# Kernel optimization log

Measured on AMD Instinct MI355X. Metric: run time of the kernel, lower is better.

## Reference

```python
import jax, jax.numpy as jnp
import numpy as np

N_QUBITS = 8
N_WORDS = 16
DEGREE = 3
N_ANSATZ_LAYERS = 2
VOCAB = 50257
EMB = 512
BATCH = 16
N_ROTS = 4 * N_QUBITS * N_ANSATZ_LAYERS  # 64
DIM = 2 ** N_QUBITS


def _ry_mat(th):
    # [[cos, -sin],[sin, cos]] on theta/2, batched over leading dim
    c = jnp.cos(th / 2).astype(jnp.complex64)
    s = jnp.sin(th / 2).astype(jnp.complex64)
    return jnp.stack([jnp.stack([c, -s], -1), jnp.stack([s, c], -1)], -2)


def _rx_mat(th):
    # [[cos, -i sin],[-i sin, cos]] on theta/2
    c = jnp.cos(th / 2).astype(jnp.complex64)
    s = jnp.sin(th / 2).astype(jnp.complex64)
    return jnp.stack([jnp.stack([c, -1j * s], -1), jnp.stack([-1j * s, c], -1)], -2)


def _apply_1q(st, M, w):
    # st: [BB, 2^n] complex, M: [BB,2,2]; wire 0 is the most-significant axis (tq convention)
    BB = st.shape[0]
    s = st.reshape(BB, 2 ** w, 2, -1)
    s = jnp.einsum('bij,bljr->blir', M, s)
    return s.reshape(BB, -1)


def _apply_ctrl(st, M, c, t, n):
    # controlled-1q gate: apply M on target t only in the control=1 subspace
    BB = st.shape[0]
    full = st.reshape((BB,) + (2,) * n)
    s0 = jnp.take(full, 0, axis=c + 1)
    s1 = jnp.take(full, 1, axis=c + 1)
    ta = (t if t < c else t - 1) + 1  # target axis after removing control axis
    s1 = jnp.moveaxis(s1, ta, -1)
    s1 = jnp.einsum('bij,b...j->b...i', M, s1)
    s1 = jnp.moveaxis(s1, -1, ta)
    return jnp.stack([s0, s1], axis=c + 1).reshape(BB, -1)


def _sim14(st, params, n, layers):
    # circuit-14 ansatz: ry ring, crx down-ring, ry ring, crx up-ring (per layer)
    idx = 0
    for _ in range(layers):
        for i in range(n):
            st = _apply_1q(st, _ry_mat(params[:, idx]), i); idx += 1
        for i in range(n - 1, -1, -1):
            st = _apply_ctrl(st, _rx_mat(params[:, idx]), i, (i + 1) % n, n); idx += 1
        for i in range(n):
            st = _apply_1q(st, _ry_mat(params[:, idx]), i); idx += 1
        for i in [n - 1] + list(range(n - 1)):
            st = _apply_ctrl(st, _rx_mat(params[:, idx]), i, (i - 1) % n, n); idx += 1
    return st


def _apply_unitaries(base, wparams, coeffs):
    # base: [B, DIM]; wparams: [B, W, N_ROTS]; coeffs: [B, W] complex -> LCU sum_w c_w U_w |psi>
    B, W = wparams.shape[0], wparams.shape[1]
    rep = jnp.repeat(base, W, axis=0)  # matches torch repeat(1,W).view(-1,DIM)
    st = _sim14(rep, wparams.reshape(B * W, -1), N_QUBITS, N_ANSATZ_LAYERS)
    return jnp.einsum('bwi,bw->bi', st.reshape(B, W, DIM), coeffs)


def _measure_xyz(st, n):
    # Pauli X/Y/Z expectations per wire; order: [x_0..x_{n-1}, y_..., z_...]
    BB = st.shape[0]
    xs, ys, zs = [], [], []
    for w in range(n):
        s = st.reshape(BB, 2 ** w, 2, -1)
        a0, a1 = s[:, :, 0, :], s[:, :, 1, :]
        cross = jnp.sum(jnp.conj(a0) * a1, axis=(1, 2))
        xs.append(2 * jnp.real(cross))
        ys.append(2 * jnp.imag(cross))
        zs.append(jnp.sum(jnp.abs(a0) ** 2 - jnp.abs(a1) ** 2, axis=(1, 2)))
    return jnp.concatenate([jnp.stack(xs, -1), jnp.stack(ys, -1), jnp.stack(zs, -1)], axis=-1)


def reference(x, embedding_W, emb2rot_W, emb2rot_b, poly_coeffs, mix_coeffs_ri, qff_params, ff1_W, ff1_b, ff2_W, ff2_b):
    B = x.shape[0]
    mix = (mix_coeffs_ri[:, 0] + 1j * mix_coeffs_ri[:, 1]).astype(jnp.complex64)
    coeffs = mix / jnp.maximum(jnp.sum(jnp.abs(mix)), 1e-12)  # L1 normalize
    coeffs = jnp.broadcast_to(coeffs[None, :], (B, N_WORDS))
    emb = embedding_W[x]                       # [B, W, EMB]
    wparams = emb @ emb2rot_W.T + emb2rot_b    # [B, W, N_ROTS]; dropout is identity in eval
    base = jnp.zeros((B, DIM), jnp.complex64).at[:, 0].set(1.0)
    acc = poly_coeffs[0] * base
    work = base
    for d in range(1, DEGREE + 1):
        work = _apply_unitaries(work, wparams, coeffs)
        acc = acc + poly_coeffs[d] * work
    mixed = acc / jnp.sum(jnp.abs(poly_coeffs))
    final_probs = jnp.linalg.norm(mixed, axis=-1)
    normed = mixed / jnp.maximum(final_probs, 1e-12)[:, None]
    qp = jnp.broadcast_to(qff_params[None, :4 * N_QUBITS], (B, 4 * N_QUBITS))  # qff uses 1 layer
    st = _sim14(normed, qp, N_QUBITS, 1)
    exps = _measure_xyz(st, N_QUBITS)          # [B, 3*n_qubits]
    h = jax.nn.relu(exps @ ff1_W.T + ff1_b)
    op = h @ ff2_W.T + ff2_b
    return op, jnp.mean(final_probs)


def setup_inputs():
    key = jax.random.key(0)
    ks = jax.random.split(key, 12)
    x = jax.random.randint(ks[0], (BATCH, N_WORDS), 0, VOCAB)
    embedding_W = jax.random.normal(ks[1], (VOCAB, EMB), jnp.float32) * 0.02
    emb2rot_W = jax.random.normal(ks[2], (N_ROTS, EMB), jnp.float32) * (1.0 / np.sqrt(EMB))
    emb2rot_b = jax.random.normal(ks[3], (N_ROTS,), jnp.float32) * 0.01
    poly_coeffs = jax.random.uniform(ks[4], (DEGREE + 1,), jnp.float32)
    mix_coeffs_ri = jax.random.uniform(ks[5], (N_WORDS, 2), jnp.float32)
    qff_params = jax.random.uniform(ks[6], (N_ROTS,), jnp.float32)
    NM = 3 * N_QUBITS
    ff1_W = jax.random.normal(ks[7], (EMB, NM), jnp.float32) * (1.0 / np.sqrt(NM))
    ff1_b = jnp.zeros((EMB,), jnp.float32)
    ff2_W = jax.random.normal(ks[8], (VOCAB, EMB), jnp.float32) * (1.0 / np.sqrt(EMB))
    ff2_b = jnp.zeros((VOCAB,), jnp.float32)
    return {"x": x, "embedding_W": embedding_W, "emb2rot_W": emb2rot_W, "emb2rot_b": emb2rot_b,
            "poly_coeffs": poly_coeffs, "mix_coeffs_ri": mix_coeffs_ri, "qff_params": qff_params,
            "ff1_W": ff1_W, "ff1_b": ff1_b, "ff2_W": ff2_W, "ff2_b": ff2_b}
```

## Files before the change

kernel.cpp:

```cpp
#include <hip/hip_runtime.h>
#include <hip/hip_bf16.h>

#define NQ 8
#define DIM 256
#define NB 16
#define NW 16
#define VOCABN 50257
#define EMBN 512

__device__ __forceinline__ float2 shfl2(float2 a, int m){
  float2 r; r.x = __shfl_xor(a.x, m, 64); r.y = __shfl_xor(a.y, m, 64); return r;
}
__device__ __forceinline__ float wave_sum(float x){
  #pragma unroll
  for (int off = 1; off < 64; off <<= 1) x += __shfl_xor(x, off, 64);
  return x;
}

__device__ __forceinline__ void ry_pair(float2& a0, float2& a1, float c, float s){
  float2 n0 = make_float2(c*a0.x - s*a1.x, c*a0.y - s*a1.y);
  float2 n1 = make_float2(s*a0.x + c*a1.x, s*a0.y + c*a1.y);
  a0 = n0; a1 = n1;
}
__device__ __forceinline__ void rx_pair(float2& a0, float2& a1, float c, float s){
  float2 n0 = make_float2(c*a0.x + s*a1.y, c*a0.y - s*a1.x);
  float2 n1 = make_float2(c*a1.x + s*a0.y, c*a1.y - s*a0.x);
  a0 = n0; a1 = n1;
}

__device__ __forceinline__ void apply_gate(float2 v[4], int lane, int kind, int cbit, int tbit,
                                           float c, float s){
  if (kind == 0){
    if (tbit == 7){ ry_pair(v[0], v[2], c, s); ry_pair(v[1], v[3], c, s); }
    else if (tbit == 6){ ry_pair(v[0], v[1], c, s); ry_pair(v[2], v[3], c, s); }
    else {
      int m = 1 << tbit;
      #pragma unroll
      for (int r = 0; r < 4; ++r){
        float2 w = shfl2(v[r], m);
        float sg = (lane & m) ? s : -s;
        v[r] = make_float2(c*v[r].x + sg*w.x, c*v[r].y + sg*w.y);
      }
    }
  } else {
    if (tbit >= 6){
      if (cbit >= 6){
        if (cbit == 7) rx_pair(v[2], v[3], c, s);
        else           rx_pair(v[1], v[3], c, s);
      } else {
        int cm = 1 << cbit;
        if (lane & cm){
          if (tbit == 7){ rx_pair(v[0], v[2], c, s); rx_pair(v[1], v[3], c, s); }
          else          { rx_pair(v[0], v[1], c, s); rx_pair(v[2], v[3], c, s); }
        }
      }
    } else {
      int m = 1 << tbit;
      if (cbit >= 6){
        int r0 = (cbit == 6) ? 1 : 2;
        float2 w0 = shfl2(v[r0], m);
        float2 w1 = shfl2(v[3], m);
        v[r0] = make_float2(c*v[r0].x + s*w0.y, c*v[r0].y - s*w0.x);
        v[3]  = make_float2(c*v[3].x  + s*w1.y, c*v[3].y  - s*w1.x);
      } else {
        int cm = 1 << cbit;
        bool act = (lane & cm) != 0;
        #pragma unroll
        for (int r = 0; r < 4; ++r){
          float2 w = shfl2(v[r], m);
          if (act) v[r] = make_float2(c*v[r].x + s*w.y, c*v[r].y - s*w.x);
        }
      }
    }
  }
}

__device__ __forceinline__ void sim32(float2 v[4], int lane, const float2* __restrict__ cs){
  constexpr int KIND[32] = {0,0,0,0,0,0,0,0, 1,1,1,1,1,1,1,1, 0,0,0,0,0,0,0,0, 1,1,1,1,1,1,1,1};
  constexpr int CB[32]   = {0,0,0,0,0,0,0,0, 0,1,2,3,4,5,6,7, 0,0,0,0,0,0,0,0, 0,7,6,5,4,3,2,1};
  constexpr int TB[32]   = {7,6,5,4,3,2,1,0, 7,0,1,2,3,4,5,6, 7,6,5,4,3,2,1,0, 1,0,7,6,5,4,3,2};
  #pragma unroll
  for (int g = 0; g < 32; ++g){
    float2 p = cs[g];
    apply_gate(v, lane, KIND[g], CB[g], TB[g], p.x, p.y);
  }
}

__device__ __forceinline__ void measure_one(const float2 v[4], int lane, int t,
                                            float& xr, float& xi, float& zz){
  xr = 0.f; xi = 0.f; zz = 0.f;
  if (t == 7){
    #pragma unroll
    for (int r = 0; r < 2; ++r){
      float2 a0 = v[r], a1 = v[r+2];
      xr += a0.x*a1.x + a0.y*a1.y;
      xi += a0.x*a1.y - a0.y*a1.x;
      zz += (a0.x*a0.x + a0.y*a0.y) - (a1.x*a1.x + a1.y*a1.y);
    }
  } else if (t == 6){
    #pragma unroll
    for (int r = 0; r < 4; r += 2){
      float2 a0 = v[r], a1 = v[r+1];
      xr += a0.x*a1.x + a0.y*a1.y;
      xi += a0.x*a1.y - a0.y*a1.x;
      zz += (a0.x*a0.x + a0.y*a0.y) - (a1.x*a1.x + a1.y*a1.y);
    }
  } else {
    int m = 1 << t;
    #pragma unroll
    for (int r = 0; r < 4; ++r){
      float2 a = v[r];
      float2 w = shfl2(a, m);
      if (!(lane & m)){
        xr += a.x*w.x + a.y*w.y;
        xi += a.x*w.y - a.y*w.x;
        zz += (a.x*a.x + a.y*a.y) - (w.x*w.x + w.y*w.y);
      }
    }
  }
  xr = wave_sum(xr); xi = wave_sum(xi); zz = wave_sum(zz);
}

__global__ __launch_bounds__(64) void k_pd1(
    const int* __restrict__ x, const float* __restrict__ embW,
    const float* __restrict__ e2rW, const float* __restrict__ e2rb,
    const float* __restrict__ mixri, const float* __restrict__ qff,
    float* __restrict__ wcs, float* __restrict__ qcs, float2* __restrict__ S1)
{
  const int p = blockIdx.x;
  const int j = threadIdx.x;
  __shared__ float2 cs[64];

  {
    const int tok = x[p];
    const float4* er = (const float4*)(embW + (size_t)tok * EMBN);
    const float4* wr = (const float4*)(e2rW + (size_t)j * EMBN);
    float acc = e2rb[j];
    #pragma unroll 4
    for (int k = 0; k < EMBN/4; ++k){
      float4 e = er[k], w4 = wr[k];
      acc += e.x*w4.x + e.y*w4.y + e.z*w4.z + e.w*w4.w;
    }
    float th = 0.5f * acc;
    float2 c2 = make_float2(cosf(th), sinf(th));
    cs[j] = c2;
    ((float2*)wcs)[p*64 + j] = c2;
    if (p == 0 && j < 32){ float t = 0.5f * qff[j]; ((float2*)qcs)[j] = make_float2(cosf(t), sinf(t)); }
  }
  __syncthreads();

  const int lane = j;
  float2 v[4];
  v[0] = make_float2(lane == 0 ? 1.f : 0.f, 0.f);
  v[1] = v[2] = v[3] = make_float2(0.f, 0.f);
  sim32(v, lane, cs);
  sim32(v, lane, cs + 32);

  float ssum = 0.f;
  #pragma unroll
  for (int i = 0; i < 16; ++i){
    float mr = mixri[2*i], mi = mixri[2*i+1];
    ssum += sqrtf(mr*mr + mi*mi);
  }
  ssum = fmaxf(ssum, 1e-12f);
  const int w = p & 15;
  const float2 coef = make_float2(mixri[2*w]/ssum, mixri[2*w+1]/ssum);
  #pragma unroll
  for (int r = 0; r < 4; ++r){
    float2 a = v[r];
    S1[p*DIM + ((r<<6) | lane)] = make_float2(coef.x*a.x - coef.y*a.y, coef.x*a.y + coef.y*a.x);
  }
}

__global__ __launch_bounds__(64) void k_deg(
    const float2* __restrict__ Sin, float2* __restrict__ Sout,
    const float* __restrict__ wcs, const float* __restrict__ mixri,
    const float* __restrict__ poly, float2* __restrict__ accs, int dprev)
{
  const int p = blockIdx.x, lane = threadIdx.x;
  const int b = p >> 4, w = p & 15;
  float2 v[4];
  v[0] = v[1] = v[2] = v[3] = make_float2(0.f, 0.f);
  const float2* base = Sin + b*NW*DIM;
  #pragma unroll
  for (int ww = 0; ww < NW; ++ww){
    #pragma unroll
    for (int r = 0; r < 4; ++r){
      float2 a = base[ww*DIM + ((r<<6) | lane)];
      v[r].x += a.x; v[r].y += a.y;
    }
  }
  if (w == 0){
    const float pd = poly[dprev];
    #pragma unroll
    for (int r = 0; r < 4; ++r){
      const int idx = (r<<6) | lane;
      float2 cur = make_float2(pd*v[r].x, pd*v[r].y);
      if (dprev == 1){
        if (idx == 0) cur.x += poly[0];
        accs[b*DIM + idx] = cur;
      } else {
        float2 old = accs[b*DIM + idx];
        accs[b*DIM + idx] = make_float2(old.x + cur.x, old.y + cur.y);
      }
    }
  }
  const float2* mycs = ((const float2*)wcs) + p*64;
  sim32(v, lane, mycs);
  sim32(v, lane, mycs + 32);
  float ssum = 0.f;
  #pragma unroll
  for (int i = 0; i < 16; ++i){
    float mr = mixri[2*i], mi = mixri[2*i+1];
    ssum += sqrtf(mr*mr + mi*mi);
  }
  ssum = fmaxf(ssum, 1e-12f);
  const float2 coef = make_float2(mixri[2*w]/ssum, mixri[2*w+1]/ssum);
  #pragma unroll
  for (int r = 0; r < 4; ++r){
    float2 a = v[r];
    Sout[p*DIM + ((r<<6) | lane)] = make_float2(coef.x*a.x - coef.y*a.y, coef.x*a.y + coef.y*a.x);
  }
}

__global__ __launch_bounds__(512) void k_final(
    const float2* __restrict__ Sin, const float2* __restrict__ accs,
    const float* __restrict__ poly, const float* __restrict__ qcs,
    const float* __restrict__ ff1W, const float* __restrict__ ff1b,
    float* __restrict__ hT, float* __restrict__ fprobs)
{
  const int b = blockIdx.x, tid = threadIdx.x;
  const int w = tid >> 6, lane = tid & 63;
  __shared__ float2 work[DIM];
  __shared__ float  red[8];
  __shared__ float  exps[24];
  __shared__ float  inv_s;
  __shared__ float  ff1_lds[EMBN*24];

  {
    const float4* f4 = (const float4*)ff1W;
    float4* d4 = (float4*)ff1_lds;
    #pragma unroll
    for (int i = 0; i < 6; ++i) d4[i*512 + tid] = f4[i*512 + tid];
  }
  const float psum = fabsf(poly[0]) + fabsf(poly[1]) + fabsf(poly[2]) + fabsf(poly[3]);
  float ssl = 0.f;
  if (tid < DIM){
    float2 s = make_float2(0.f, 0.f);
    const float2* base = Sin + b*NW*DIM;
    #pragma unroll
    for (int ww = 0; ww < NW; ++ww){ float2 a = base[ww*DIM + tid]; s.x += a.x; s.y += a.y; }
    float2 ac = accs[b*DIM + tid];
    const float p3 = poly[3];
    s = make_float2((ac.x + p3*s.x)/psum, (ac.y + p3*s.y)/psum);
    work[tid] = s;
    ssl = s.x*s.x + s.y*s.y;
  }
  ssl = wave_sum(ssl);
  if (lane == 0) red[w] = ssl;
  __syncthreads();
  if (tid == 0){
    float fp = sqrtf(red[0] + red[1] + red[2] + red[3]);
    fprobs[b] = fp;
    inv_s = 1.f / fmaxf(fp, 1e-12f);
  }
  __syncthreads();
  {
    const float inv = inv_s;
    float2 v[4];
    #pragma unroll
    for (int r = 0; r < 4; ++r){
      float2 m = work[(r<<6) | lane];
      v[r] = make_float2(m.x*inv, m.y*inv);
    }
    sim32(v, lane, (const float2*)qcs);
    float xr, xi, zz;
    measure_one(v, lane, 7 - w, xr, xi, zz);
    if (lane == 0){ exps[w] = 2.f*xr; exps[8+w] = 2.f*xi; exps[16+w] = zz; }
  }
  __syncthreads();
  float a = ff1b[tid];
  const float* wr = ff1_lds + tid*24;
  #pragma unroll
  for (int m2 = 0; m2 < 24; ++m2) a += exps[m2]*wr[m2];
  hT[tid*NB + b] = fmaxf(a, 0.f);
}

__global__ __launch_bounds__(256) void k_out(
    const float* __restrict__ hT, const float* __restrict__ ff2W,
    const float* __restrict__ ff2b, const float* __restrict__ fprobs,
    float* __restrict__ out)
{
  __shared__ float4 hs[2048];
  const int tid = threadIdx.x;
  const int q = tid >> 6;
  const int lane = tid & 63;

  if (blockIdx.x == 0 && tid == 0){
    float s = 0.f;
    #pragma unroll
    for (int i = 0; i < 16; ++i) s += fprobs[i];
    out[(size_t)NB*VOCABN] = s * (1.f/16.f);
  }

  {
    const float4* hT4 = (const float4*)hT;
    #pragma unroll
    for (int i = 0; i < 8; ++i) hs[i*256 + tid] = hT4[i*256 + tid];
  }
  __syncthreads();

  const int base = blockIdx.x * 128;
  const int r0 = base + lane;
  const int r1 = r0 + 64;
  const int rc0 = min(r0, VOCABN-1);
  const int rc1 = min(r1, VOCABN-1);

  float4 acc0[4], acc1[4];
  #pragma unroll
  for (int i = 0; i < 4; ++i){ acc0[i] = make_float4(0,0,0,0); acc1[i] = make_float4(0,0,0,0); }

  const float4* w0 = (const float4*)(ff2W + (size_t)rc0 * EMBN) + q*32;
  const float4* w1 = (const float4*)(ff2W + (size_t)rc1 * EMBN) + q*32;

  #pragma unroll 4
  for (int c = 0; c < 32; ++c){
    float4 wa = w0[c];
    float4 wb = w1[c];
    const int k0 = (q*128 + c*4) << 2;
    #pragma unroll
    for (int kk = 0; kk < 4; ++kk){
      const float wka = (kk==0) ? wa.x : (kk==1) ? wa.y : (kk==2) ? wa.z : wa.w;
      const float wkb = (kk==0) ? wb.x : (kk==1) ? wb.y : (kk==2) ? wb.z : wb.w;
      #pragma unroll
      for (int bq = 0; bq < 4; ++bq){
        float4 hh = hs[k0 + kk*4 + bq];
        acc0[bq].x += wka*hh.x; acc0[bq].y += wka*hh.y;
        acc0[bq].z += wka*hh.z; acc0[bq].w += wka*hh.w;
        acc1[bq].x += wkb*hh.x; acc1[bq].y += wkb*hh.y;
        acc1[bq].z += wkb*hh.z; acc1[bq].w += wkb*hh.w;
      }
    }
  }
  __syncthreads();

  float* redf = (float*)hs;
  if (q > 0){
    float* dst = redf + (q-1)*2112 + lane*33;
    #pragma unroll
    for (int bq = 0; bq < 4; ++bq){
      dst[bq*4+0] = acc0[bq].x; dst[bq*4+1] = acc0[bq].y;
      dst[bq*4+2] = acc0[bq].z; dst[bq*4+3] = acc0[bq].w;
      dst[16+bq*4+0] = acc1[bq].x; dst[16+bq*4+1] = acc1[bq].y;
      dst[16+bq*4+2] = acc1[bq].z; dst[16+bq*4+3] = acc1[bq].w;
    }
  }
  __syncthreads();
  if (q == 0){
    #pragma unroll
    for (int qq = 0; qq < 3; ++qq){
      const float* src = redf + qq*2112 + lane*33;
      #pragma unroll
      for (int bq = 0; bq < 4; ++bq){
        acc0[bq].x += src[bq*4+0]; acc0[bq].y += src[bq*4+1];
        acc0[bq].z += src[bq*4+2]; acc0[bq].w += src[bq*4+3];
        acc1[bq].x += src[16+bq*4+0]; acc1[bq].y += src[16+bq*4+1];
        acc1[bq].z += src[16+bq*4+2]; acc1[bq].w += src[16+bq*4+3];
      }
    }
    if (r0 < VOCABN){
      const float bias = ff2b[r0];
      #pragma unroll
      for (int bq = 0; bq < 4; ++bq){
        out[(size_t)(bq*4+0)*VOCABN + r0] = acc0[bq].x + bias;
        out[(size_t)(bq*4+1)*VOCABN + r0] = acc0[bq].y + bias;
        out[(size_t)(bq*4+2)*VOCABN + r0] = acc0[bq].z + bias;
        out[(size_t)(bq*4+3)*VOCABN + r0] = acc0[bq].w + bias;
      }
    }
    if (r1 < VOCABN){
      const float bias = ff2b[r1];
      #pragma unroll
      for (int bq = 0; bq < 4; ++bq){
        out[(size_t)(bq*4+0)*VOCABN + r1] = acc1[bq].x + bias;
        out[(size_t)(bq*4+1)*VOCABN + r1] = acc1[bq].y + bias;
        out[(size_t)(bq*4+2)*VOCABN + r1] = acc1[bq].z + bias;
        out[(size_t)(bq*4+3)*VOCABN + r1] = acc1[bq].w + bias;
      }
    }
  }
}

extern "C" void kernel_launch(void* const* d_in, const int* in_sizes, int n_in,
                              void* d_out, int out_size, void* d_ws, size_t ws_size,
                              hipStream_t stream)
{
  const int*   x     = (const int*)  d_in[0];
  const float* embW  = (const float*)d_in[1];
  const float* e2rW  = (const float*)d_in[2];
  const float* e2rb  = (const float*)d_in[3];
  const float* poly  = (const float*)d_in[4];
  const float* mixri = (const float*)d_in[5];
  const float* qff   = (const float*)d_in[6];
  const float* ff1W  = (const float*)d_in[7];
  const float* ff1b  = (const float*)d_in[8];
  const float* ff2W  = (const float*)d_in[9];
  const float* ff2b  = (const float*)d_in[10];
  float* out = (float*)d_out;
  float* ws  = (float*)d_ws;

  float*  wcs    = ws;
  float*  qcs    = ws + 32768;
  float*  hT     = ws + 32832;
  float*  fprobs = ws + 41024;
  float2* accs   = (float2*)(ws + 41040);
  float2* S1     = (float2*)(ws + 49232);
  float2* S2     = (float2*)(ws + 180304);

  k_pd1  <<<256, 64, 0, stream>>>(x, embW, e2rW, e2rb, mixri, qff, wcs, qcs, S1);
  k_deg  <<<256, 64, 0, stream>>>(S1, S2, wcs, mixri, poly, accs, 1);
  k_deg  <<<256, 64, 0, stream>>>(S2, S1, wcs, mixri, poly, accs, 2);
  k_final<<<NB, 512, 0, stream>>>(S1, accs, poly, qcs, ff1W, ff1b, hT, fprobs);
  k_out  <<<(VOCABN + 127)/128, 256, 0, stream>>>(hT, ff2W, ff2b, fprobs, out);
}
```

Before: 290.0 us.

## Compute vocab projection with bf16 MFMA tiles instead of FP32 FMA

Rewrites the final vocab projection kernel so that each wave computes a 16-row vocab tile for all 16 batch rows using the bf16 16x16x32 MFMA instruction. The hidden activations are now written as bf16 in batch-major order and loaded straight into register fragments, so the LDS staging and the cross-wave reduction go away. The fp32 weights are converted to bf16 on the fly, which lowers the precision of the large output GEMM. The kernel still reads the fp32 weight matrix, so it probably stays bound by memory bandwidth.

After: 278.0 us. 4.1% less time.

```diff
diff --git a/kernel.cpp b/kernel.cpp
--- a/kernel.cpp
+++ b/kernel.cpp
@@ -7,6 +7,10 @@
 #define NW 16
 #define VOCABN 50257
 #define EMBN 512
+#define NTILES ((VOCABN + 15) / 16)
+
+typedef __attribute__((ext_vector_type(8))) short short8;
+typedef __attribute__((ext_vector_type(4))) float f32x4;
 
 __device__ __forceinline__ float2 shfl2(float2 a, int m){
   float2 r; r.x = __shfl_xor(a.x, m, 64); r.y = __shfl_xor(a.y, m, 64); return r;
@@ -15,6 +19,10 @@
   #pragma unroll
   for (int off = 1; off < 64; off <<= 1) x += __shfl_xor(x, off, 64);
   return x;
+}
+__device__ __forceinline__ short f2bf(float f){
+  __hip_bfloat16 h = __float2bfloat16(f);
+  return __builtin_bit_cast(short, h);
 }
 
 __device__ __forceinline__ void ry_pair(float2& a0, float2& a1, float c, float s){
@@ -227,7 +235,7 @@
     const float2* __restrict__ Sin, const float2* __restrict__ accs,
     const float* __restrict__ poly, const float* __restrict__ qcs,
     const float* __restrict__ ff1W, const float* __restrict__ ff1b,
-    float* __restrict__ hT, float* __restrict__ fprobs)
+    __hip_bfloat16* __restrict__ hbf, float* __restrict__ fprobs)
 {
   const int b = blockIdx.x, tid = threadIdx.x;
   const int w = tid >> 6, lane = tid & 63;
@@ -283,18 +291,17 @@
   const float* wr = ff1_lds + tid*24;
   #pragma unroll
   for (int m2 = 0; m2 < 24; ++m2) a += exps[m2]*wr[m2];
-  hT[tid*NB + b] = fmaxf(a, 0.f);
+  hbf[b*EMBN + tid] = __float2bfloat16(fmaxf(a, 0.f));
 }
 
 __global__ __launch_bounds__(256) void k_out(
-    const float* __restrict__ hT, const float* __restrict__ ff2W,
+    const __hip_bfloat16* __restrict__ hbf, const float* __restrict__ ff2W,
     const float* __restrict__ ff2b, const float* __restrict__ fprobs,
     float* __restrict__ out)
 {
-  __shared__ float4 hs[2048];
   const int tid = threadIdx.x;
-  const int q = tid >> 6;
-  const int lane = tid & 63;
+  const int w = tid >> 6, lane = tid & 63;
+  const int tile = blockIdx.x*4 + w;
 
   if (blockIdx.x == 0 && tid == 0){
     float s = 0.f;
@@ -303,91 +310,38 @@
     out[(size_t)NB*VOCABN] = s * (1.f/16.f);
   }
 
+  const int n = lane & 15;
+  const int quad = lane >> 4;
+
+  short8 bfrag[16];
   {
-    const float4* hT4 = (const float4*)hT;
-    #pragma unroll
-    for (int i = 0; i < 8; ++i) hs[i*256 + tid] = hT4[i*256 + tid];
-  }
-  __syncthreads();
-
-  const int base = blockIdx.x * 128;
-  const int r0 = base + lane;
-  const int r1 = r0 + 64;
-  const int rc0 = min(r0, VOCABN-1);
-  const int rc1 = min(r1, VOCABN-1);
-
-  float4 acc0[4], acc1[4];
-  #pragma unroll
-  for (int i = 0; i < 4; ++i){ acc0[i] = make_float4(0,0,0,0); acc1[i] = make_float4(0,0,0,0); }
-
-  const float4* w0 = (const float4*)(ff2W + (size_t)rc0 * EMBN) + q*32;
-  const float4* w1 = (const float4*)(ff2W + (size_t)rc1 * EMBN) + q*32;
-
-  #pragma unroll 4
-  for (int c = 0; c < 32; ++c){
-    float4 wa = w0[c];
-    float4 wb = w1[c];
-    const int k0 = (q*128 + c*4) << 2;
-    #pragma unroll
-    for (int kk = 0; kk < 4; ++kk){
-      const float wka = (kk==0) ? wa.x : (kk==1) ? wa.y : (kk==2) ? wa.z : wa.w;
-      const float wkb = (kk==0) ? wb.x : (kk==1) ? wb.y : (kk==2) ? wb.z : wb.w;
-      #pragma unroll
-      for (int bq = 0; bq < 4; ++bq){
-        float4 hh = hs[k0 + kk*4 + bq];
-        acc0[bq].x += wka*hh.x; acc0[bq].y += wka*hh.y;
-        acc0[bq].z += wka*hh.z; acc0[bq].w += wka*hh.w;
-        acc1[bq].x += wkb*hh.x; acc1[bq].y += wkb*hh.y;
-        acc1[bq].z += wkb*hh.z; acc1[bq].w += wkb*hh.w;
-      }
-    }
-  }
-  __syncthreads();
-
-  float* redf = (float*)hs;
-  if (q > 0){
-    float* dst = redf + (q-1)*2112 + lane*33;
-    #pragma unroll
-    for (int bq = 0; bq < 4; ++bq){
-      dst[bq*4+0] = acc0[bq].x; dst[bq*4+1] = acc0[bq].y;
-      dst[bq*4+2] = acc0[bq].z; dst[bq*4+3] = acc0[bq].w;
-      dst[16+bq*4+0] = acc1[bq].x; dst[16+bq*4+1] = acc1[bq].y;
-      dst[16+bq*4+2] = acc1[bq].z; dst[16+bq*4+3] = acc1[bq].w;
-    }
-  }
-  __syncthreads();
-  if (q == 0){
-    #pragma unroll
-    for (int qq = 0; qq < 3; ++qq){
-      const float* src = redf + qq*2112 + lane*33;
-      #pragma unroll
-      for (int bq = 0; bq < 4; ++bq){
-        acc0[bq].x += src[bq*4+0]; acc0[bq].y += src[bq*4+1];
-        acc0[bq].z += src[bq*4+2]; acc0[bq].w += src[bq*4+3];
-        acc1[bq].x += src[16+bq*4+0]; acc1[bq].y += src[16+bq*4+1];
-        acc1[bq].z += src[16+bq*4+2]; acc1[bq].w += src[16+bq*4+3];
-      }
-    }
-    if (r0 < VOCABN){
-      const float bias = ff2b[r0];
-      #pragma unroll
-      for (int bq = 0; bq < 4; ++bq){
-        out[(size_t)(bq*4+0)*VOCABN + r0] = acc0[bq].x + bias;
-        out[(size_t)(bq*4+1)*VOCABN + r0] = acc0[bq].y + bias;
-        out[(size_t)(bq*4+2)*VOCABN + r0] = acc0[bq].z + bias;
-        out[(size_t)(bq*4+3)*VOCABN + r0] = acc0[bq].w + bias;
-      }
-    }
-    if (r1 < VOCABN){
-      const float bias = ff2b[r1];
-      #pragma unroll
-      for (int bq = 0; bq < 4; ++bq){
-        out[(size_t)(bq*4+0)*VOCABN + r1] = acc1[bq].x + bias;
-        out[(size_t)(bq*4+1)*VOCABN + r1] = acc1[bq].y + bias;
-        out[(size_t)(bq*4+2)*VOCABN + r1] = acc1[bq].z + bias;
-        out[(size_t)(bq*4+3)*VOCABN + r1] = acc1[bq].w + bias;
-      }
-    }
+    const short* hb = (const short*)hbf + n*EMBN;
+    #pragma unroll
+    for (int f = 0; f < 16; ++f)
+      bfrag[f] = *(const short8*)(hb + f*32 + quad*8);
+  }
+
+  if (tile >= NTILES) return;
+  const int tbase = tile * 16;
+  int row = tbase + n; if (row > VOCABN-1) row = VOCABN-1;
+  const float* ar = ff2W + (size_t)row * EMBN + quad*8;
+
+  f32x4 acc = {0.f, 0.f, 0.f, 0.f};
+  #pragma unroll
+  for (int f = 0; f < 16; ++f){
+    float4 a0 = *(const float4*)(ar + f*32);
+    float4 a1 = *(const float4*)(ar + f*32 + 4);
+    short8 af;
+    af[0] = f2bf(a0.x); af[1] = f2bf(a0.y); af[2] = f2bf(a0.z); af[3] = f2bf(a0.w);
+    af[4] = f2bf(a1.x); af[5] = f2bf(a1.y); af[6] = f2bf(a1.z); af[7] = f2bf(a1.w);
+    acc = __builtin_amdgcn_mfma_f32_16x16x32_bf16(af, bfrag[f], acc, 0, 0, 0);
+  }
+
+  #pragma unroll
+  for (int r = 0; r < 4; ++r){
+    const int v = tbase + quad*4 + r;
+    if (v < VOCABN)
+      out[(size_t)n*VOCABN + v] = acc[r] + ff2b[v];
   }
 }
 
@@ -411,15 +365,15 @@
 
   float*  wcs    = ws;
   float*  qcs    = ws + 32768;
-  float*  hT     = ws + 32832;
-  float*  fprobs = ws + 41024;
-  float2* accs   = (float2*)(ws + 41040);
-  float2* S1     = (float2*)(ws + 49232);
-  float2* S2     = (float2*)(ws + 180304);
+  __hip_bfloat16* hbf = (__hip_bfloat16*)(ws + 32832);
+  float*  fprobs = ws + 36928;
+  float2* accs   = (float2*)(ws + 36944);
+  float2* S1     = (float2*)(ws + 45136);
+  float2* S2     = (float2*)(ws + 176208);
 
   k_pd1  <<<256, 64, 0, stream>>>(x, embW, e2rW, e2rb, mixri, qff, wcs, qcs, S1);
   k_deg  <<<256, 64, 0, stream>>>(S1, S2, wcs, mixri, poly, accs, 1);
   k_deg  <<<256, 64, 0, stream>>>(S2, S1, wcs, mixri, poly, accs, 2);
-  k_final<<<NB, 512, 0, stream>>>(S1, accs, poly, qcs, ff1W, ff1b, hT, fprobs);
-  k_out  <<<(VOCABN + 127)/128, 256, 0, stream>>>(hT, ff2W, ff2b, fprobs, out);
-}
+  k_final<<<NB, 512, 0, stream>>>(S1, accs, poly, qcs, ff1W, ff1b, hbf, fprobs);
+  k_out  <<<(NTILES + 3)/4, 256, 0, stream>>>(hbf, ff2W, ff2b, fprobs, out);
+}
```
